# Kernel optimization log

Measured on AMD Instinct MI355X. Metric: run time of the kernel, lower is better.

Reference implementation:

```python
import jax, jax.numpy as jnp
import numpy as np

N = 100000   # nodes
E = 1600000  # edges
IN_DIM = 64
OUT_DIM = 32


def setup_inputs() -> dict:
    key = jax.random.key(0)
    ks = jax.random.split(key, 9)
    x = jax.random.normal(ks[0], (N, IN_DIM), dtype=jnp.float32)
    edge_index = jax.random.randint(ks[1], (2, E), 0, N, dtype=jnp.int64)
    edge_weight = jax.random.uniform(ks[2], (E,), dtype=jnp.float32)
    def glorot(k, fan_in, fan_out):
        s = jnp.sqrt(6.0 / (fan_in + fan_out)).astype(jnp.float32)
        return jax.random.uniform(k, (fan_in, fan_out), jnp.float32, -s, s)
    W1 = glorot(ks[3], IN_DIM, 2 * IN_DIM)
    b1 = jnp.zeros((2 * IN_DIM,), jnp.float32)
    W2 = glorot(ks[4], 2 * IN_DIM, 2 * OUT_DIM)
    b2 = jnp.zeros((2 * OUT_DIM,), jnp.float32)
    W3 = glorot(ks[5], 2 * OUT_DIM, OUT_DIM)
    b3 = jnp.zeros((OUT_DIM,), jnp.float32)
    return {"x": x, "edge_index": edge_index, "edge_weight": edge_weight,
            "W1": W1, "b1": b1, "W2": W2, "b2": b2, "W3": W3, "b3": b3,
            "sigmoid": True}


def reference(x, edge_index, edge_weight, W1, b1, W2, b2, W3, b3, sigmoid):
    n = x.shape[0]
    row, col = edge_index[0], edge_index[1]  # source -> target
    # GCN symmetric normalization with implicit self-loops of weight 1
    deg = jax.ops.segment_sum(edge_weight, col, num_segments=n) + 1.0  # [N]
    dinv = jax.lax.rsqrt(deg)
    norm_e = dinv[row] * edge_weight * dinv[col]  # [E]
    norm_self = dinv * dinv                        # [N] self-loop coeff

    def gcn(h, W, b):
        h = h @ W  # linear transform first (PyG GCNConv order)
        agg = jax.ops.segment_sum(h[row] * norm_e[:, None], col, num_segments=n)
        return agg + h * norm_self[:, None] + b

    h = gcn(x, W1, b1)
    h = gcn(h, W2, b2)
    h = gcn(h, W3, b3)
    return jax.nn.sigmoid(h) if sigmoid else h
```

## Files before the change

kernel.cpp:

```cpp
#include <hip/hip_runtime.h>
#include <hip/hip_fp16.h>
#include <math.h>


#define EPB 4096
#define MAXBKT 512

__global__ __launch_bounds__(256) void hist1_kernel(const int* __restrict__ ei,
                                                    int* __restrict__ hist1,
                                                    int nbkt, int nblk1, int E) {
    __shared__ int lh[MAXBKT];
    int tid = threadIdx.x;
    for (int b = tid; b < nbkt; b += 256) lh[b] = 0;
    __syncthreads();
    int base = blockIdx.x * EPB;
    #pragma unroll
    for (int j = 0; j < EPB / 256; ++j) {
        int e = base + j * 256 + tid;
        if (e < E) atomicAdd(&lh[ei[E + e] >> 8], 1);
    }
    __syncthreads();
    for (int b = tid; b < nbkt; b += 256)
        hist1[(size_t)b * nblk1 + blockIdx.x] = lh[b];
}

__global__ void scan_block_kernel(const int* __restrict__ counts, int* __restrict__ outp,
                                  int* __restrict__ bsums, int n) {
    __shared__ int s[256];
    int tid = threadIdx.x;
    int i = blockIdx.x * 256 + tid;
    int v = (i < n) ? counts[i] : 0;
    s[tid] = v;
    __syncthreads();
    for (int off = 1; off < 256; off <<= 1) {
        int t = (tid >= off) ? s[tid - off] : 0;
        __syncthreads();
        s[tid] += t;
        __syncthreads();
    }
    if (i < n) outp[i] = s[tid] - v;
    if (tid == 255) bsums[blockIdx.x] = s[255];
}

__global__ void scan_bsums_kernel(int* __restrict__ bsums, int nb) {
    __shared__ int s[1024];
    int tid = threadIdx.x;
    int v = (tid < nb) ? bsums[tid] : 0;
    s[tid] = v;
    __syncthreads();
    for (int off = 1; off < 1024; off <<= 1) {
        int t = (tid >= off) ? s[tid - off] : 0;
        __syncthreads();
        s[tid] += t;
        __syncthreads();
    }
    if (tid < nb) bsums[tid] = s[tid] - v;
}

__global__ void scan_add_kernel(int* __restrict__ outp, const int* __restrict__ bsums,
                                int n, int E) {
    int i = blockIdx.x * 256 + threadIdx.x;
    if (i < n) outp[i] += bsums[i >> 8];
    if (i == n) outp[n] = E;
}

__global__ __launch_bounds__(256) void bucket_scatter_kernel(const int* __restrict__ ei,
                                                             const float* __restrict__ ew,
                                                             const int* __restrict__ scan1,
                                                             int2* __restrict__ tmp,
                                                             int nbkt, int nblk1, int E) {
    __shared__ int cur[MAXBKT];
    int tid = threadIdx.x;
    for (int b = tid; b < nbkt; b += 256)
        cur[b] = scan1[(size_t)b * nblk1 + blockIdx.x];
    __syncthreads();
    int base = blockIdx.x * EPB;
    #pragma unroll
    for (int j = 0; j < EPB / 256; ++j) {
        int e = base + j * 256 + tid;
        if (e < E) {
            int s = ei[e];
            int d = ei[E + e];
            float w = ew[e];
            int pos = atomicAdd(&cur[d >> 8], 1);
            tmp[pos] = make_int2(s | ((d & 255) << 20), __float_as_int(w));
        }
    }
}

__global__ __launch_bounds__(256) void bucket_build_kernel(const int* __restrict__ scan1,
                                                           const int2* __restrict__ tmp,
                                                           int* __restrict__ rowptr,
                                                           int2* __restrict__ csr,
                                                           float* __restrict__ dinv,
                                                           int nblk1, int N, int E) {
    __shared__ int s[256];
    __shared__ int cur[256];
    __shared__ float wsum[256];
    int b = blockIdx.x;
    int tid = threadIdx.x;
    int beg = scan1[(size_t)b * nblk1];
    int end = scan1[(size_t)(b + 1) * nblk1];

    s[tid] = 0;
    wsum[tid] = 0.f;
    __syncthreads();
    for (int i = beg + tid; i < end; i += 256) {
        int2 r = tmp[i];
        int dl = r.x >> 20;
        atomicAdd(&s[dl], 1);
        atomicAdd(&wsum[dl], __int_as_float(r.y));
    }
    __syncthreads();
    int myc = s[tid];
    for (int off = 1; off < 256; off <<= 1) {
        int t = (tid >= off) ? s[tid - off] : 0;
        __syncthreads();
        s[tid] += t;
        __syncthreads();
    }
    int excl = s[tid] - myc;
    cur[tid] = excl;
    int node = b * 256 + tid;
    if (node <= N) rowptr[node] = beg + excl;
    if (node < N)  dinv[node] = rsqrtf(1.0f + wsum[tid]);
    __syncthreads();
    for (int i = beg + tid; i < end; i += 256) {
        int2 r = tmp[i];
        int dl = r.x >> 20;
        int pos = beg + atomicAdd(&cur[dl], 1);
        csr[pos] = make_int2(r.x & 0xFFFFF, r.y);
    }
}

__global__ void nrm_s1_kernel(const float* __restrict__ dinv, const int* __restrict__ rowptr,
                              int2* __restrict__ csr, float* __restrict__ s1, int n) {
    int v = blockIdx.x * 256 + threadIdx.x;
    if (v >= n) return;
    float dv = dinv[v];
    float acc = dv * dv;
    int beg = rowptr[v], end = rowptr[v + 1];
    for (int i = beg; i < end; ++i) {
        int2 rec = csr[i];
        float nm = dv * __int_as_float(rec.y) * dinv[rec.x];
        acc += nm;
        rec.y = __float_as_int(nm);
        csr[i] = rec;
    }
    s1[v] = acc;
}

__global__ __launch_bounds__(256) void compose1_kernel(const float* __restrict__ W1,
                                                       const float* __restrict__ b1,
                                                       const float* __restrict__ W2,
                                                       float* __restrict__ U) {
    __shared__ float s[256];
    int r = blockIdx.x;
    int tid = threadIdx.x;
    int c = tid & 63;
    int q = tid >> 6;
    const float* arow = (r < 64) ? &W1[r * 128] : b1;
    float acc = 0.f;
    #pragma unroll 8
    for (int k = q * 32; k < q * 32 + 32; ++k)
        acc += arow[k] * W2[k * 64 + c];
    s[tid] = acc;
    __syncthreads();
    if (q == 0)
        U[r * 64 + c] = s[c] + s[c + 64] + s[c + 128] + s[c + 192];
}

__global__ __launch_bounds__(256) void compose2_kernel(const float* __restrict__ U,
                                                       const float* __restrict__ b2,
                                                       const float* __restrict__ W3,
                                                       float* __restrict__ Wc,
                                                       float* __restrict__ c1,
                                                       float* __restrict__ c2) {
    __shared__ float s[256];
    int r = blockIdx.x;
    int tid = threadIdx.x;
    int c = tid & 31;
    int o = tid >> 5;
    const float* arow = (r < 65) ? &U[r * 64] : b2;
    float acc = 0.f;
    #pragma unroll
    for (int k = o * 8; k < o * 8 + 8; ++k)
        acc += arow[k] * W3[k * 32 + c];
    s[tid] = acc;
    __syncthreads();
    if (o == 0) {
        float v = 0.f;
        #pragma unroll
        for (int j = 0; j < 8; ++j) v += s[c + j * 32];
        if (r < 64) Wc[r * 32 + c] = v;
        else if (r == 64) c1[c] = v;
        else c2[c] = v;
    }
}

template <int K, int D>
__global__ __launch_bounds__(256) void gemm_kernel(const float* __restrict__ X,
                                                   const float* __restrict__ W,
                                                   __half* __restrict__ T, int n) {
    constexpr int NB = 64;
    __shared__ float sW[K * D];
    __shared__ float sX[NB * K];
    int tid = threadIdx.x;
    int base = blockIdx.x * NB;
    int nthis = n - base;
    if (nthis > NB) nthis = NB;

    for (int i = tid * 4; i < K * D; i += 256 * 4)
        *(float4*)&sW[i] = *(const float4*)&W[i];
    for (int i = tid * 4; i < nthis * K; i += 256 * 4)
        *(float4*)&sX[i] = *(const float4*)&X[(size_t)base * K + i];
    __syncthreads();

    constexpr int C4 = D / 4;
    constexpr int NG = 256 / C4;
    int c4 = tid % C4;
    int ng = tid / C4;
    for (int nl = ng; nl < nthis; nl += NG) {
        const float* xr = &sX[nl * K];
        float4 acc = {0.f, 0.f, 0.f, 0.f};
        #pragma unroll
        for (int k = 0; k < K; ++k) {
            float a = xr[k];
            float4 wv = *(const float4*)&sW[k * D + c4 * 4];
            acc.x += a * wv.x; acc.y += a * wv.y;
            acc.z += a * wv.z; acc.w += a * wv.w;
        }
        __half2 h0 = __floats2half2_rn(acc.x, acc.y);
        __half2 h1 = __floats2half2_rn(acc.z, acc.w);
        uint2 u = { *(unsigned*)&h0, *(unsigned*)&h1 };
        *(uint2*)&T[(size_t)(base + nl) * D + c4 * 4] = u;
    }
}

template <int PHASE>
__global__ __launch_bounds__(256) void agg32_kernel(const __half* __restrict__ T,
                                                    const float* __restrict__ dinv,
                                                    const int* __restrict__ rowptr,
                                                    const int2* __restrict__ csr,
                                                    const float* __restrict__ s1,
                                                    float* __restrict__ s2,
                                                    const float* __restrict__ c1,
                                                    const float* __restrict__ c2,
                                                    const float* __restrict__ b3,
                                                    void* __restrict__ outp, int n) {
    int c4 = threadIdx.x & 7;
    int node = blockIdx.x * 32 + (threadIdx.x >> 3);
    if (node >= n) return;

    float di = dinv[node];
    float ns = di * di;
    uint2 tu = *(const uint2*)&T[(size_t)node * 32 + c4 * 4];
    float2 t0 = __half22float2(*(__half2*)&tu.x);
    float2 t1 = __half22float2(*(__half2*)&tu.y);
    float4 acc = { t0.x * ns, t0.y * ns, t1.x * ns, t1.y * ns };
    float sacc = (PHASE == 0) ? ns * s1[node] : 0.f;

    int beg = rowptr[node];
    int end = rowptr[node + 1];
    int i = beg;
    for (; i + 4 <= end; i += 4) {
        int2 r0 = csr[i];
        int2 r1 = csr[i + 1];
        int2 r2 = csr[i + 2];
        int2 r3 = csr[i + 3];
        uint2 g0 = *(const uint2*)&T[(size_t)r0.x * 32 + c4 * 4];
        uint2 g1 = *(const uint2*)&T[(size_t)r1.x * 32 + c4 * 4];
        uint2 g2 = *(const uint2*)&T[(size_t)r2.x * 32 + c4 * 4];
        uint2 g3 = *(const uint2*)&T[(size_t)r3.x * 32 + c4 * 4];
        float w0 = __int_as_float(r0.y);
        float w1 = __int_as_float(r1.y);
        float w2 = __int_as_float(r2.y);
        float w3 = __int_as_float(r3.y);
        float2 a0 = __half22float2(*(__half2*)&g0.x);
        float2 a1 = __half22float2(*(__half2*)&g0.y);
        float2 b0 = __half22float2(*(__half2*)&g1.x);
        float2 b1 = __half22float2(*(__half2*)&g1.y);
        float2 e0 = __half22float2(*(__half2*)&g2.x);
        float2 e1 = __half22float2(*(__half2*)&g2.y);
        float2 f0 = __half22float2(*(__half2*)&g3.x);
        float2 f1 = __half22float2(*(__half2*)&g3.y);
        acc.x += w0 * a0.x + w1 * b0.x + w2 * e0.x + w3 * f0.x;
        acc.y += w0 * a0.y + w1 * b0.y + w2 * e0.y + w3 * f0.y;
        acc.z += w0 * a1.x + w1 * b1.x + w2 * e1.x + w3 * f1.x;
        acc.w += w0 * a1.y + w1 * b1.y + w2 * e1.y + w3 * f1.y;
        if (PHASE == 0) sacc += w0 * s1[r0.x] + w1 * s1[r1.x] + w2 * s1[r2.x] + w3 * s1[r3.x];
    }
    for (; i < end; ++i) {
        int2 r0 = csr[i];
        uint2 g0 = *(const uint2*)&T[(size_t)r0.x * 32 + c4 * 4];
        float w0 = __int_as_float(r0.y);
        float2 a0 = __half22float2(*(__half2*)&g0.x);
        float2 a1 = __half22float2(*(__half2*)&g0.y);
        acc.x += w0 * a0.x;
        acc.y += w0 * a0.y;
        acc.z += w0 * a1.x;
        acc.w += w0 * a1.y;
        if (PHASE == 0) sacc += w0 * s1[r0.x];
    }

    if (PHASE == 0 && c4 == 0) s2[node] = sacc;

    if (PHASE == 2) {
        float a = s2[node], b = s1[node];
        float4 c1v = *(const float4*)&c1[c4 * 4];
        float4 c2v = *(const float4*)&c2[c4 * 4];
        float4 b3v = *(const float4*)&b3[c4 * 4];
        acc.x += a * c1v.x + b * c2v.x + b3v.x;
        acc.y += a * c1v.y + b * c2v.y + b3v.y;
        acc.z += a * c1v.z + b * c2v.z + b3v.z;
        acc.w += a * c1v.w + b * c2v.w + b3v.w;
        acc.x = 1.f / (1.f + __expf(-acc.x));
        acc.y = 1.f / (1.f + __expf(-acc.y));
        acc.z = 1.f / (1.f + __expf(-acc.z));
        acc.w = 1.f / (1.f + __expf(-acc.w));
        *(float4*)&((float*)outp)[(size_t)node * 32 + c4 * 4] = acc;
    } else {
        __half2 h0 = __floats2half2_rn(acc.x, acc.y);
        __half2 h1 = __floats2half2_rn(acc.z, acc.w);
        uint2 u = { *(unsigned*)&h0, *(unsigned*)&h1 };
        *(uint2*)&((__half*)outp)[(size_t)node * 32 + c4 * 4] = u;
    }
}

extern "C" void kernel_launch(void* const* d_in, const int* in_sizes, int n_in,
                              void* d_out, int out_size, void* d_ws, size_t ws_size,
                              hipStream_t stream) {
    const float* x  = (const float*)d_in[0];
    const int*   ei = (const int*)d_in[1];
    const float* ew = (const float*)d_in[2];
    const float* W1 = (const float*)d_in[3];
    const float* b1 = (const float*)d_in[4];
    const float* W2 = (const float*)d_in[5];
    const float* b2 = (const float*)d_in[6];
    const float* W3 = (const float*)d_in[7];
    const float* b3 = (const float*)d_in[8];
    float* out = (float*)d_out;

    const int N = in_sizes[0] / 64;
    const int E = in_sizes[2];

    const int nbkt  = (N + 255) >> 8;
    const int nblk1 = (E + EPB - 1) / EPB;
    const int nscan = nbkt * nblk1;

    auto a16 = [](size_t v) { return (v + 15) & ~(size_t)15; };
    char* p = (char*)d_ws;
    int*    hist1  = (int*)p;    p += a16((size_t)nscan * 4);
    int*    scan1  = (int*)p;    p += a16((size_t)(nscan + 1) * 4);
    int*    bsums  = (int*)p;    p += a16((size_t)1024 * 4);
    int2*   tmp    = (int2*)p;   p += a16((size_t)E * 8);
    int*    rowptr = (int*)p;    p += a16((size_t)(N + 1) * 4);
    int2*   csr    = (int2*)p;   p += a16((size_t)E * 8);
    float*  dinv   = (float*)p;  p += a16((size_t)N * 4);
    float*  s1     = (float*)p;  p += a16((size_t)N * 4);
    float*  s2     = (float*)p;  p += a16((size_t)N * 4);
    float*  Uc     = (float*)p;  p += a16((size_t)65 * 64 * 4);
    float*  Wc     = (float*)p;  p += a16((size_t)64 * 32 * 4);
    float*  c1     = (float*)p;  p += a16((size_t)32 * 4);
    float*  c2     = (float*)p;  p += a16((size_t)32 * 4);
    __half* y      = (__half*)p; p += a16((size_t)N * 32 * 2);
    __half* z      = (__half*)p; p += a16((size_t)N * 32 * 2);

    const int nbN = (N + 255) / 256;
    const int scanBlocks = (nscan + 255) / 256;

    hist1_kernel<<<nblk1, 256, 0, stream>>>(ei, hist1, nbkt, nblk1, E);
    scan_block_kernel<<<scanBlocks, 256, 0, stream>>>(hist1, scan1, bsums, nscan);
    scan_bsums_kernel<<<1, 1024, 0, stream>>>(bsums, scanBlocks);
    scan_add_kernel<<<(nscan + 1 + 255) / 256, 256, 0, stream>>>(scan1, bsums, nscan, E);
    bucket_scatter_kernel<<<nblk1, 256, 0, stream>>>(ei, ew, scan1, tmp, nbkt, nblk1, E);
    bucket_build_kernel<<<nbkt, 256, 0, stream>>>(scan1, tmp, rowptr, csr, dinv, nblk1, N, E);

    nrm_s1_kernel<<<nbN, 256, 0, stream>>>(dinv, rowptr, csr, s1, N);

    compose1_kernel<<<65, 256, 0, stream>>>(W1, b1, W2, Uc);
    compose2_kernel<<<66, 256, 0, stream>>>(Uc, b2, W3, Wc, c1, c2);
    gemm_kernel<64, 32><<<(N + 63) / 64, 256, 0, stream>>>(x, Wc, y, N);

    const int aggGrid = (N + 31) / 32;
    agg32_kernel<0><<<aggGrid, 256, 0, stream>>>(y, dinv, rowptr, csr, s1, s2, c1, c2, b3, z, N);
    agg32_kernel<1><<<aggGrid, 256, 0, stream>>>(z, dinv, rowptr, csr, s1, s2, c1, c2, b3, y, N);
    agg32_kernel<2><<<aggGrid, 256, 0, stream>>>(y, dinv, rowptr, csr, s1, s2, c1, c2, b3, out, N);
}
```

Baseline: 213.5 us.

## Split each row's neighbors by source half to improve gather cache locality

Within each CSR row, edges are now ordered by whether the source node lies in the first or second half of the node range, and a rowmid pointer is recorded. Each aggregation layer is split into two passes: one gathers only low-half sources into an fp32 partial buffer, the second gathers high-half sources and finishes the layer. The aim is for each pass's random gather working set (half of the fp16 feature table) to fit better in cache. The s2 scalar computation moves into its own kernel. In exchange this adds three launches, an extra N×32 fp32 partial write and read per layer, and a second pass over the CSR.

Result: slower. 239.6 us (+12.2%).

```diff
diff --git a/kernel.cpp b/kernel.cpp
--- a/kernel.cpp
+++ b/kernel.cpp
@@ -91,45 +91,55 @@
 __global__ __launch_bounds__(256) void bucket_build_kernel(const int* __restrict__ scan1,
                                                            const int2* __restrict__ tmp,
                                                            int* __restrict__ rowptr,
+                                                           int* __restrict__ rowmid,
                                                            int2* __restrict__ csr,
                                                            float* __restrict__ dinv,
-                                                           int nblk1, int N, int E) {
-    __shared__ int s[256];
-    __shared__ int cur[256];
+                                                           int nblk1, int N, int E, int H) {
+    __shared__ int s[512];
+    __shared__ int cur[512];
     __shared__ float wsum[256];
     int b = blockIdx.x;
     int tid = threadIdx.x;
     int beg = scan1[(size_t)b * nblk1];
     int end = scan1[(size_t)(b + 1) * nblk1];
 
-    s[tid] = 0;
+    s[tid] = 0; s[tid + 256] = 0;
     wsum[tid] = 0.f;
     __syncthreads();
     for (int i = beg + tid; i < end; i += 256) {
         int2 r = tmp[i];
         int dl = r.x >> 20;
-        atomicAdd(&s[dl], 1);
+        int src = r.x & 0xFFFFF;
+        int half = (src >= H) ? 1 : 0;
+        atomicAdd(&s[dl * 2 + half], 1);
         atomicAdd(&wsum[dl], __int_as_float(r.y));
     }
     __syncthreads();
-    int myc = s[tid];
-    for (int off = 1; off < 256; off <<= 1) {
-        int t = (tid >= off) ? s[tid - off] : 0;
-        __syncthreads();
-        s[tid] += t;
-        __syncthreads();
-    }
-    int excl = s[tid] - myc;
-    cur[tid] = excl;
+    for (int off = 1; off < 512; off <<= 1) {
+        int a = (tid >= off) ? s[tid - off] : 0;
+        int c = (tid + 256 >= off) ? s[tid + 256 - off] : 0;
+        __syncthreads();
+        s[tid] += a; s[tid + 256] += c;
+        __syncthreads();
+    }
+    int exA = (tid == 0) ? 0 : s[2 * tid - 1];
+    int exB = s[2 * tid];
     int node = b * 256 + tid;
-    if (node <= N) rowptr[node] = beg + excl;
-    if (node < N)  dinv[node] = rsqrtf(1.0f + wsum[tid]);
+    if (node <= N) rowptr[node] = beg + exA;
+    if (node < N) {
+        rowmid[node] = beg + exB;
+        dinv[node] = rsqrtf(1.0f + wsum[tid]);
+    }
+    cur[2 * tid] = beg + exA;
+    cur[2 * tid + 1] = beg + exB;
     __syncthreads();
     for (int i = beg + tid; i < end; i += 256) {
         int2 r = tmp[i];
         int dl = r.x >> 20;
-        int pos = beg + atomicAdd(&cur[dl], 1);
-        csr[pos] = make_int2(r.x & 0xFFFFF, r.y);
+        int src = r.x & 0xFFFFF;
+        int half = (src >= H) ? 1 : 0;
+        int pos = atomicAdd(&cur[dl * 2 + half], 1);
+        csr[pos] = make_int2(src, r.y);
     }
 }
 
@@ -148,6 +158,21 @@
         csr[i] = rec;
     }
     s1[v] = acc;
+}
+
+__global__ void s2_kernel(const float* __restrict__ dinv, const int* __restrict__ rowptr,
+                          const int2* __restrict__ csr, const float* __restrict__ s1,
+                          float* __restrict__ s2, int n) {
+    int v = blockIdx.x * 256 + threadIdx.x;
+    if (v >= n) return;
+    float dv = dinv[v];
+    float acc = dv * dv * s1[v];
+    int beg = rowptr[v], end = rowptr[v + 1];
+    for (int i = beg; i < end; ++i) {
+        int2 rec = csr[i];
+        acc += __int_as_float(rec.y) * s1[rec.x];
+    }
+    s2[v] = acc;
 }
 
 __global__ __launch_bounds__(256) void compose1_kernel(const float* __restrict__ W1,
@@ -237,32 +262,9 @@
     }
 }
 
-template <int PHASE>
-__global__ __launch_bounds__(256) void agg32_kernel(const __half* __restrict__ T,
-                                                    const float* __restrict__ dinv,
-                                                    const int* __restrict__ rowptr,
-                                                    const int2* __restrict__ csr,
-                                                    const float* __restrict__ s1,
-                                                    float* __restrict__ s2,
-                                                    const float* __restrict__ c1,
-                                                    const float* __restrict__ c2,
-                                                    const float* __restrict__ b3,
-                                                    void* __restrict__ outp, int n) {
-    int c4 = threadIdx.x & 7;
-    int node = blockIdx.x * 32 + (threadIdx.x >> 3);
-    if (node >= n) return;
-
-    float di = dinv[node];
-    float ns = di * di;
-    uint2 tu = *(const uint2*)&T[(size_t)node * 32 + c4 * 4];
-    float2 t0 = __half22float2(*(__half2*)&tu.x);
-    float2 t1 = __half22float2(*(__half2*)&tu.y);
-    float4 acc = { t0.x * ns, t0.y * ns, t1.x * ns, t1.y * ns };
-    float sacc = (PHASE == 0) ? ns * s1[node] : 0.f;
-
-    int beg = rowptr[node];
-    int end = rowptr[node + 1];
-    int i = beg;
+__device__ __forceinline__ void gather_acc(const __half* __restrict__ T, int c4,
+                                           const int2* __restrict__ csr,
+                                           int i, int end, float4& acc) {
     for (; i + 4 <= end; i += 4) {
         int2 r0 = csr[i];
         int2 r1 = csr[i + 1];
@@ -288,7 +290,6 @@
         acc.y += w0 * a0.y + w1 * b0.y + w2 * e0.y + w3 * f0.y;
         acc.z += w0 * a1.x + w1 * b1.x + w2 * e1.x + w3 * f1.x;
         acc.w += w0 * a1.y + w1 * b1.y + w2 * e1.y + w3 * f1.y;
-        if (PHASE == 0) sacc += w0 * s1[r0.x] + w1 * s1[r1.x] + w2 * s1[r2.x] + w3 * s1[r3.x];
     }
     for (; i < end; ++i) {
         int2 r0 = csr[i];
@@ -300,12 +301,51 @@
         acc.y += w0 * a0.y;
         acc.z += w0 * a1.x;
         acc.w += w0 * a1.y;
-        if (PHASE == 0) sacc += w0 * s1[r0.x];
-    }
-
-    if (PHASE == 0 && c4 == 0) s2[node] = sacc;
-
-    if (PHASE == 2) {
+    }
+}
+
+__global__ __launch_bounds__(256) void aggA_kernel(const __half* __restrict__ T,
+                                                   const int* __restrict__ rowptr,
+                                                   const int* __restrict__ rowmid,
+                                                   const int2* __restrict__ csr,
+                                                   float* __restrict__ P, int n) {
+    int c4 = threadIdx.x & 7;
+    int node = blockIdx.x * 32 + (threadIdx.x >> 3);
+    if (node >= n) return;
+    float4 acc = {0.f, 0.f, 0.f, 0.f};
+    gather_acc(T, c4, csr, rowptr[node], rowmid[node], acc);
+    *(float4*)&P[(size_t)node * 32 + c4 * 4] = acc;
+}
+
+template <bool FINAL>
+__global__ __launch_bounds__(256) void aggB_kernel(const __half* __restrict__ T,
+                                                   const float* __restrict__ P,
+                                                   const float* __restrict__ dinv,
+                                                   const int* __restrict__ rowptr,
+                                                   const int* __restrict__ rowmid,
+                                                   const int2* __restrict__ csr,
+                                                   const float* __restrict__ s1,
+                                                   const float* __restrict__ s2,
+                                                   const float* __restrict__ c1,
+                                                   const float* __restrict__ c2,
+                                                   const float* __restrict__ b3,
+                                                   void* __restrict__ outp, int n) {
+    int c4 = threadIdx.x & 7;
+    int node = blockIdx.x * 32 + (threadIdx.x >> 3);
+    if (node >= n) return;
+
+    float di = dinv[node];
+    float ns = di * di;
+    float4 acc = *(const float4*)&P[(size_t)node * 32 + c4 * 4];
+    uint2 tu = *(const uint2*)&T[(size_t)node * 32 + c4 * 4];
+    float2 t0 = __half22float2(*(__half2*)&tu.x);
+    float2 t1 = __half22float2(*(__half2*)&tu.y);
+    acc.x += t0.x * ns; acc.y += t0.y * ns;
+    acc.z += t1.x * ns; acc.w += t1.y * ns;
+
+    gather_acc(T, c4, csr, rowmid[node], rowptr[node + 1], acc);
+
+    if (FINAL) {
         float a = s2[node], b = s1[node];
         float4 c1v = *(const float4*)&c1[c4 * 4];
         float4 c2v = *(const float4*)&c2[c4 * 4];
@@ -343,6 +383,7 @@
 
     const int N = in_sizes[0] / 64;
     const int E = in_sizes[2];
+    const int H = N / 2;
 
     const int nbkt  = (N + 255) >> 8;
     const int nblk1 = (E + EPB - 1) / EPB;
@@ -355,6 +396,7 @@
     int*    bsums  = (int*)p;    p += a16((size_t)1024 * 4);
     int2*   tmp    = (int2*)p;   p += a16((size_t)E * 8);
     int*    rowptr = (int*)p;    p += a16((size_t)(N + 1) * 4);
+    int*    rowmid = (int*)p;    p += a16((size_t)N * 4);
     int2*   csr    = (int2*)p;   p += a16((size_t)E * 8);
     float*  dinv   = (float*)p;  p += a16((size_t)N * 4);
     float*  s1     = (float*)p;  p += a16((size_t)N * 4);
@@ -363,6 +405,7 @@
     float*  Wc     = (float*)p;  p += a16((size_t)64 * 32 * 4);
     float*  c1     = (float*)p;  p += a16((size_t)32 * 4);
     float*  c2     = (float*)p;  p += a16((size_t)32 * 4);
+    float*  P      = (float*)p;  p += a16((size_t)N * 32 * 4);
     __half* y      = (__half*)p; p += a16((size_t)N * 32 * 2);
     __half* z      = (__half*)p; p += a16((size_t)N * 32 * 2);
 
@@ -374,16 +417,20 @@
     scan_bsums_kernel<<<1, 1024, 0, stream>>>(bsums, scanBlocks);
     scan_add_kernel<<<(nscan + 1 + 255) / 256, 256, 0, stream>>>(scan1, bsums, nscan, E);
     bucket_scatter_kernel<<<nblk1, 256, 0, stream>>>(ei, ew, scan1, tmp, nbkt, nblk1, E);
-    bucket_build_kernel<<<nbkt, 256, 0, stream>>>(scan1, tmp, rowptr, csr, dinv, nblk1, N, E);
+    bucket_build_kernel<<<nbkt, 256, 0, stream>>>(scan1, tmp, rowptr, rowmid, csr, dinv, nblk1, N, E, H);
 
     nrm_s1_kernel<<<nbN, 256, 0, stream>>>(dinv, rowptr, csr, s1, N);
+    s2_kernel<<<nbN, 256, 0, stream>>>(dinv, rowptr, csr, s1, s2, N);
 
     compose1_kernel<<<65, 256, 0, stream>>>(W1, b1, W2, Uc);
     compose2_kernel<<<66, 256, 0, stream>>>(Uc, b2, W3, Wc, c1, c2);
     gemm_kernel<64, 32><<<(N + 63) / 64, 256, 0, stream>>>(x, Wc, y, N);
 
     const int aggGrid = (N + 31) / 32;
-    agg32_kernel<0><<<aggGrid, 256, 0, stream>>>(y, dinv, rowptr, csr, s1, s2, c1, c2, b3, z, N);
-    agg32_kernel<1><<<aggGrid, 256, 0, stream>>>(z, dinv, rowptr, csr, s1, s2, c1, c2, b3, y, N);
-    agg32_kernel<2><<<aggGrid, 256, 0, stream>>>(y, dinv, rowptr, csr, s1, s2, c1, c2, b3, out, N);
-}
+    aggA_kernel<<<aggGrid, 256, 0, stream>>>(y, rowptr, rowmid, csr, P, N);
+    aggB_kernel<false><<<aggGrid, 256, 0, stream>>>(y, P, dinv, rowptr, rowmid, csr, s1, s2, c1, c2, b3, z, N);
+    aggA_kernel<<<aggGrid, 256, 0, stream>>>(z, rowptr, rowmid, csr, P, N);
+    aggB_kernel<false><<<aggGrid, 256, 0, stream>>>(z, P, dinv, rowptr, rowmid, csr, s1, s2, c1, c2, b3, y, N);
+    aggA_kernel<<<aggGrid, 256, 0, stream>>>(y, rowptr, rowmid, csr, P, N);
+    aggB_kernel<true ><<<aggGrid, 256, 0, stream>>>(y, P, dinv, rowptr, rowmid, csr, s1, s2, c1, c2, b3, out, N);
+}
```
